# Kernel tuning notes

Measured on AMD Instinct MI355X. Metric: run time of the kernel, lower is better.

## Reference

```python
import jax, jax.numpy as jnp
import numpy as np

N = 50000      # nodes
E = 800000     # edges (before self loops)
IN = 128       # input feature dim
HID = 64       # hidden channels per head
H = 4          # heads
OUT = 1        # final out channels
D1 = H * HID   # 256, concat feature dim
NEG_SLOPE = 0.2


def _p(k, shape):
    return jax.random.normal(k, shape, jnp.float32) * 0.1


def setup_inputs() -> dict:
    key = jax.random.key(0)
    ks = jax.random.split(key, 32)
    inp = {
        "x": jax.random.normal(ks[0], (N, IN), jnp.float32),
        "edge_index": jax.random.randint(ks[1], (2, E), 0, N, dtype=jnp.int32),
        "batch": jnp.zeros((N,), jnp.int32),
    }
    # layer 0: GATConv(IN -> HID, heads=H, concat) ; Linear(IN -> H*HID)
    inp["cW0"] = _p(ks[2], (IN, H * HID)); inp["cas0"] = _p(ks[3], (H, HID))
    inp["cad0"] = _p(ks[4], (H, HID));     inp["cb0"] = jnp.zeros((D1,), jnp.float32)
    inp["lW0"] = _p(ks[5], (IN, D1));      inp["lb0"] = jnp.zeros((D1,), jnp.float32)
    # layer 1: GATConv(D1 -> HID, heads=H, concat) ; Linear(D1 -> D1)
    inp["cW1"] = _p(ks[6], (D1, H * HID)); inp["cas1"] = _p(ks[7], (H, HID))
    inp["cad1"] = _p(ks[8], (H, HID));     inp["cb1"] = jnp.zeros((D1,), jnp.float32)
    inp["lW1"] = _p(ks[9], (D1, D1));      inp["lb1"] = jnp.zeros((D1,), jnp.float32)
    # layer 2: GATConv(D1 -> OUT, heads=H, concat=False -> mean) ; Linear(D1 -> OUT)
    inp["cW2"] = _p(ks[10], (D1, H * OUT)); inp["cas2"] = _p(ks[11], (H, OUT))
    inp["cad2"] = _p(ks[12], (H, OUT));     inp["cb2"] = jnp.zeros((OUT,), jnp.float32)
    inp["lW2"] = _p(ks[13], (D1, OUT));     inp["lb2"] = jnp.zeros((OUT,), jnp.float32)
    return inp


def gat_conv(x, W, att_src, att_dst, bias, src, dst, out_c, concat):
    """PyG-style GATConv with self loops already included in (src, dst)."""
    n = x.shape[0]
    xl = (x @ W).reshape(n, H, out_c)                  # [N,H,C]
    a_s = (xl * att_src).sum(-1)                       # [N,H]
    a_d = (xl * att_dst).sum(-1)                       # [N,H]
    e = jax.nn.leaky_relu(a_s[src] + a_d[dst], NEG_SLOPE)   # [Et,H]
    # numerically stable segment softmax over destination nodes
    e_max = jax.ops.segment_max(e, dst, num_segments=n)
    ex = jnp.exp(e - e_max[dst])
    denom = jax.ops.segment_sum(ex, dst, num_segments=n)
    alpha = ex / (denom[dst] + 1e-16)                  # [Et,H]
    msg = xl[src] * alpha[..., None]                   # [Et,H,C]
    out = jax.ops.segment_sum(msg, dst, num_segments=n)  # [N,H,C]
    out = out.reshape(n, H * out_c) if concat else out.mean(axis=1)
    return out + bias


def _forward(x, edge_index,
             cW0, cas0, cad0, cb0, lW0, lb0,
             cW1, cas1, cad1, cb1, lW1, lb1,
             cW2, cas2, cad2, cb2, lW2, lb2):
    n = x.shape[0]
    loop = jnp.arange(n, dtype=edge_index.dtype)
    src = jnp.concatenate([edge_index[0], loop])
    dst = jnp.concatenate([edge_index[1], loop])
    h = jax.nn.elu(gat_conv(x, cW0, cas0, cad0, cb0, src, dst, HID, True) + (x @ lW0 + lb0))
    h = jax.nn.elu(gat_conv(h, cW1, cas1, cad1, cb1, src, dst, HID, True) + (h @ lW1 + lb1))
    return gat_conv(h, cW2, cas2, cad2, cb2, src, dst, OUT, False) + (h @ lW2 + lb2)


def reference(x, edge_index, batch,
              cW0, cas0, cad0, cb0, lW0, lb0,
              cW1, cas1, cad1, cb1, lW1, lb1,
              cW2, cas2, cad2, cb2, lW2, lb2):
    return _forward(x, edge_index,
                    cW0, cas0, cad0, cb0, lW0, lb0,
                    cW1, cas1, cad1, cb1, lW1, lb1,
                    cW2, cas2, cad2, cb2, lW2, lb2)
```

## Files before the change

kernel.cpp:

```cpp
#include <hip/hip_runtime.h>
#include <cstddef>
#include <cstdint>

#define NN 50000
#define EE 800000
#define ET_ (EE + NN)

typedef __attribute__((ext_vector_type(8))) short bf16x8;
typedef __attribute__((ext_vector_type(4))) float f32x4;

__device__ __forceinline__ float lrelu_(float x) { return x > 0.f ? x : 0.2f * x; }
__device__ __forceinline__ float elu_(float x)   { return x > 0.f ? x : (__expf(x) - 1.f); }
__device__ __forceinline__ short f2bf(float f) {
    unsigned u = __float_as_uint(f);
    unsigned r = (u + 0x7fffu + ((u >> 16) & 1u)) >> 16;
    return (short)r;
}
__device__ __forceinline__ float bflo(unsigned u) { return __uint_as_float(u << 16); }
__device__ __forceinline__ float bfhi(unsigned u) { return __uint_as_float(u & 0xffff0000u); }

#define GL16(gp, lp) __builtin_amdgcn_global_load_lds( \
    (const __attribute__((address_space(1))) unsigned int*)(gp), \
    (__attribute__((address_space(3))) unsigned int*)(lp), 16, 0, 0)


__global__ __launch_bounds__(256) void degree_k(const int* __restrict__ ei, int* __restrict__ deg) {
    int e = blockIdx.x * blockDim.x + threadIdx.x;
    if (e >= ET_) return;
    int d = (e < EE) ? ei[EE + e] : (e - EE);
    atomicAdd(&deg[d], 1);
}

__global__ __launch_bounds__(1024) void alloc_scan(const int* __restrict__ deg, int* __restrict__ rowptr,
                                                   int* __restrict__ gcnt, int n) {
    __shared__ int s[1024];
    __shared__ int basesh;
    int tid = threadIdx.x;
    int gid = blockIdx.x * 1024 + tid;
    int v = (gid < n) ? deg[gid] : 0;
    s[tid] = v;
    __syncthreads();
    for (int off = 1; off < 1024; off <<= 1) {
        int t = (tid >= off) ? s[tid - off] : 0;
        __syncthreads();
        s[tid] += t;
        __syncthreads();
    }
    if (tid == 1023) basesh = atomicAdd(gcnt, s[1023]);
    __syncthreads();
    if (gid < n) rowptr[gid] = basesh + s[tid] - v;
}

__global__ __launch_bounds__(256) void scatter_k(const int* __restrict__ ei,
                                                 const int* __restrict__ rowptr,
                                                 int* __restrict__ cursor,
                                                 int* __restrict__ csr_src) {
    int e = blockIdx.x * blockDim.x + threadIdx.x;
    if (e >= ET_) return;
    int s, d;
    if (e < EE) { s = ei[e]; d = ei[EE + e]; } else { s = e - EE; d = e - EE; }
    int pos = atomicAdd(&cursor[d], 1);
    csr_src[rowptr[d] + pos] = s;
}


__global__ __launch_bounds__(256) void prep_all(const float* __restrict__ x,
                                                const float* __restrict__ cW0, const float* __restrict__ lW0,
                                                const float* __restrict__ cW1, const float* __restrict__ lW1,
                                                short* __restrict__ xb, short* __restrict__ Wt0,
                                                short* __restrict__ Wt1) {
    int i = blockIdx.x * 256 + threadIdx.x;
    if (i < 1600000) {
        float4 v = *(const float4*)(x + (size_t)i * 4);
        short4 o;
        o.x = f2bf(v.x); o.y = f2bf(v.y); o.z = f2bf(v.z); o.w = f2bf(v.w);
        *(short4*)(xb + (size_t)i * 4) = o;
        return;
    }
    i -= 1600000;
    if (i < 512 * 128) {
        int n = i >> 7, k = i & 127;
        float v = (n < 256) ? cW0[k * 256 + n] : lW0[k * 256 + (n - 256)];
        Wt0[i] = f2bf(v);
        return;
    }
    i -= 512 * 128;
    if (i < 512 * 256) {
        int n = i >> 8, k = i & 255;
        float v = (n < 256) ? cW1[k * 256 + n] : lW1[k * 256 + (n - 256)];
        Wt1[i] = f2bf(v);
    }
}


__global__ __launch_bounds__(256) void gemm_bf16(const short* __restrict__ A,
                                                 const short* __restrict__ Wt,
                                                 const float* __restrict__ biasLin,
                                                 short* __restrict__ XLb,
                                                 short* __restrict__ Hlinb,
                                                 int M, int K) {
    __shared__ short As[128 * 32];
    __shared__ short Bs[128 * 32];
    const int tid = threadIdx.x;
    const int lane = tid & 63;
    const int wid = tid >> 6;
    const int bm = blockIdx.x * 128;
    const int col0 = blockIdx.y * 128;
    const int wr = wid >> 1, wc = wid & 1;

    f32x4 acc[4][4];
#pragma unroll
    for (int i = 0; i < 4; ++i)
#pragma unroll
        for (int j = 0; j < 4; ++j) acc[i][j] = (f32x4){0.f, 0.f, 0.f, 0.f};

    const int lrow = lane & 15, lk = lane >> 4;

    for (int k0 = 0; k0 < K; k0 += 32) {
#pragma unroll
        for (int it = 0; it < 2; ++it) {
            const int flat = tid + it * 256;
            const int row = flat >> 2, slot = flat & 3;
            const int ss = slot ^ (row & 3);
            int ar = bm + row; ar = (ar < M) ? ar : (M - 1);
            GL16(A + (size_t)ar * K + k0 + ss * 8, As + flat * 8);
            GL16(Wt + (size_t)(col0 + row) * K + k0 + ss * 8, Bs + flat * 8);
        }
        __syncthreads();
        bf16x8 af[4], bfr[4];
#pragma unroll
        for (int mi = 0; mi < 4; ++mi) {
            const int r = wr * 64 + mi * 16 + lrow;
            af[mi] = *(const bf16x8*)(As + (r * 4 + (lk ^ (r & 3))) * 8);
        }
#pragma unroll
        for (int ni = 0; ni < 4; ++ni) {
            const int c = wc * 64 + ni * 16 + lrow;
            bfr[ni] = *(const bf16x8*)(Bs + (c * 4 + (lk ^ (c & 3))) * 8);
        }
#pragma unroll
        for (int mi = 0; mi < 4; ++mi)
#pragma unroll
            for (int ni = 0; ni < 4; ++ni)
                acc[mi][ni] = __builtin_amdgcn_mfma_f32_16x16x32_bf16(af[mi], bfr[ni], acc[mi][ni], 0, 0, 0);
        __syncthreads();
    }

    const int lrow4 = (lane >> 4) * 4;
    const bool isLin = (col0 >= 256);
#pragma unroll
    for (int mi = 0; mi < 4; ++mi) {
#pragma unroll
        for (int ni = 0; ni < 4; ++ni) {
            const int col = col0 + wc * 64 + ni * 16 + (lane & 15);
#pragma unroll
            for (int rr = 0; rr < 4; ++rr) {
                const int grow = bm + wr * 64 + mi * 16 + lrow4 + rr;
                if (grow < M) {
                    float v = acc[mi][ni][rr];
                    if (isLin) {
                        const int c = col - 256;
                        Hlinb[(size_t)grow * 256 + c] = f2bf(v + biasLin[c]);
                    } else {
                        XLb[(size_t)grow * 256 + col] = f2bf(v);
                    }
                }
            }
        }
    }
}


__global__ __launch_bounds__(256) void attn_prep(const short* __restrict__ XLb,
                                                 const float* __restrict__ cas,
                                                 const float* __restrict__ cad,
                                                 float* __restrict__ AS,
                                                 float* __restrict__ AD, int n_nodes) {
    int n = (blockIdx.x * blockDim.x + threadIdx.x) >> 6;
    int lane = threadIdx.x & 63;
    if (n >= n_nodes) return;
    uint2 q = *(const uint2*)(XLb + (size_t)n * 256 + lane * 4);
    float x0 = bflo(q.x), x1 = bfhi(q.x);
    float x2 = bflo(q.y), x3 = bfhi(q.y);
    float4 sv = *(const float4*)(cas + lane * 4);
    float4 dv = *(const float4*)(cad + lane * 4);
    float ps = x0 * sv.x + x1 * sv.y + x2 * sv.z + x3 * sv.w;
    float pd = x0 * dv.x + x1 * dv.y + x2 * dv.z + x3 * dv.w;
#pragma unroll
    for (int off = 1; off < 16; off <<= 1) {
        ps += __shfl_xor(ps, off);
        pd += __shfl_xor(pd, off);
    }
    if ((lane & 15) == 0) {
        AS[n * 4 + (lane >> 4)] = ps;
        AD[n * 4 + (lane >> 4)] = pd;
    }
}


__global__ __launch_bounds__(256) void gat_agg(const short* __restrict__ XLb,
                                               const float* __restrict__ AS,
                                               const float* __restrict__ AD,
                                               const int* __restrict__ rowptr,
                                               const int* __restrict__ degarr,
                                               const int* __restrict__ csr_src,
                                               const float* __restrict__ cb,
                                               const short* __restrict__ Hlinb,
                                               short* __restrict__ Hb, int n_nodes) {
    __shared__ int   sIdx[4][64];
    __shared__ float sExT[4][4][72];

    const int tid = threadIdx.x;
    const int lane = tid & 63;
    const int w = tid >> 6;
    const int n = blockIdx.x * 4 + w;
    if (n >= n_nodes) return;

    const int rs = rowptr[n];
    const int deg = degarr[n];
    const float4 ad4 = *(const float4*)(AD + n * 4);

    float m0 = -1e30f, m1 = -1e30f, m2 = -1e30f, m3 = -1e30f;
    for (int base = 0; base < deg; base += 64) {
        int idx = base + lane;
        if (idx < deg) {
            int s = csr_src[rs + idx];
            float4 a = *(const float4*)(AS + s * 4);
            m0 = fmaxf(m0, lrelu_(a.x + ad4.x));
            m1 = fmaxf(m1, lrelu_(a.y + ad4.y));
            m2 = fmaxf(m2, lrelu_(a.z + ad4.z));
            m3 = fmaxf(m3, lrelu_(a.w + ad4.w));
        }
    }
#pragma unroll
    for (int off = 32; off > 0; off >>= 1) {
        m0 = fmaxf(m0, __shfl_xor(m0, off));
        m1 = fmaxf(m1, __shfl_xor(m1, off));
        m2 = fmaxf(m2, __shfl_xor(m2, off));
        m3 = fmaxf(m3, __shfl_xor(m3, off));
    }

    const int half = lane >> 5;
    const int l32 = lane & 31;
    const int ch0 = l32 * 8;
    const int h = l32 >> 3;

    float4 acc0 = make_float4(0.f, 0.f, 0.f, 0.f);
    float4 acc1 = make_float4(0.f, 0.f, 0.f, 0.f);
    float d0 = 0.f, d1 = 0.f, d2 = 0.f, d3 = 0.f;

    for (int base = 0; base < deg; base += 64) {
        int cnt = deg - base; if (cnt > 64) cnt = 64;
        int idx = base + lane;
        int sv = 0;
        float e0 = 0.f, e1 = 0.f, e2 = 0.f, e3 = 0.f;
        if (idx < deg) {
            sv = csr_src[rs + idx];
            float4 a = *(const float4*)(AS + sv * 4);
            e0 = __expf(lrelu_(a.x + ad4.x) - m0);
            e1 = __expf(lrelu_(a.y + ad4.y) - m1);
            e2 = __expf(lrelu_(a.z + ad4.z) - m2);
            e3 = __expf(lrelu_(a.w + ad4.w) - m3);
        }
        sIdx[w][lane] = sv;
        sExT[w][0][lane] = e0; sExT[w][1][lane] = e1;
        sExT[w][2][lane] = e2; sExT[w][3][lane] = e3;
        d0 += e0; d1 += e1; d2 += e2; d3 += e3;
        __builtin_amdgcn_wave_barrier();

        int cpad = (cnt + 1) & ~1;
        for (int j = 0; j < cpad; j += 2) {
            int jj = j + half;
            int s = sIdx[w][jj];
            float e = sExT[w][h][jj];
            const uint4 q = *(const uint4*)(XLb + (size_t)s * 256 + ch0);
            acc0.x += e * bflo(q.x); acc0.y += e * bfhi(q.x);
            acc0.z += e * bflo(q.y); acc0.w += e * bfhi(q.y);
            acc1.x += e * bflo(q.z); acc1.y += e * bfhi(q.z);
            acc1.z += e * bflo(q.w); acc1.w += e * bfhi(q.w);
        }
        __builtin_amdgcn_wave_barrier();
    }

    acc0.x += __shfl_xor(acc0.x, 32); acc0.y += __shfl_xor(acc0.y, 32);
    acc0.z += __shfl_xor(acc0.z, 32); acc0.w += __shfl_xor(acc0.w, 32);
    acc1.x += __shfl_xor(acc1.x, 32); acc1.y += __shfl_xor(acc1.y, 32);
    acc1.z += __shfl_xor(acc1.z, 32); acc1.w += __shfl_xor(acc1.w, 32);
#pragma unroll
    for (int off = 32; off > 0; off >>= 1) {
        d0 += __shfl_xor(d0, off); d1 += __shfl_xor(d1, off);
        d2 += __shfl_xor(d2, off); d3 += __shfl_xor(d3, off);
    }
    float den = (h == 0) ? d0 : (h == 1) ? d1 : (h == 2) ? d2 : d3;
    float inv = 1.f / (den + 1e-16f);

    if (lane < 32) {
        size_t o = (size_t)n * 256 + ch0;
        uint4 hq = *(const uint4*)(Hlinb + o);
        float4 cba = *(const float4*)(cb + ch0);
        float4 cbb = *(const float4*)(cb + ch0 + 4);
        float v0 = elu_(acc0.x * inv + cba.x + bflo(hq.x));
        float v1 = elu_(acc0.y * inv + cba.y + bfhi(hq.x));
        float v2 = elu_(acc0.z * inv + cba.z + bflo(hq.y));
        float v3 = elu_(acc0.w * inv + cba.w + bfhi(hq.y));
        float v4 = elu_(acc1.x * inv + cbb.x + bflo(hq.z));
        float v5 = elu_(acc1.y * inv + cbb.y + bfhi(hq.z));
        float v6 = elu_(acc1.z * inv + cbb.z + bflo(hq.w));
        float v7 = elu_(acc1.w * inv + cbb.w + bfhi(hq.w));
        uint4 ov;
        ov.x = (unsigned)(unsigned short)f2bf(v0) | ((unsigned)(unsigned short)f2bf(v1) << 16);
        ov.y = (unsigned)(unsigned short)f2bf(v2) | ((unsigned)(unsigned short)f2bf(v3) << 16);
        ov.z = (unsigned)(unsigned short)f2bf(v4) | ((unsigned)(unsigned short)f2bf(v5) << 16);
        ov.w = (unsigned)(unsigned short)f2bf(v6) | ((unsigned)(unsigned short)f2bf(v7) << 16);
        *(uint4*)(Hb + o) = ov;
    }
}


__global__ __launch_bounds__(256) void l2_prep(const short* __restrict__ Hin,
                                               const float* __restrict__ cW2,
                                               const float* __restrict__ lW2,
                                               const float* __restrict__ lb2,
                                               float* __restrict__ XL2,
                                               float* __restrict__ LIN2, int n_nodes) {
    int n = (blockIdx.x * blockDim.x + threadIdx.x) >> 6;
    int lane = threadIdx.x & 63;
    if (n >= n_nodes) return;
    uint2 q = *(const uint2*)(Hin + (size_t)n * 256 + lane * 4);
    float hk0 = bflo(q.x), hk1 = bfhi(q.x);
    float hk2 = bflo(q.y), hk3 = bfhi(q.y);
    int k = lane * 4;
    float4 w0 = *(const float4*)(cW2 + (k + 0) * 4);
    float4 w1 = *(const float4*)(cW2 + (k + 1) * 4);
    float4 w2 = *(const float4*)(cW2 + (k + 2) * 4);
    float4 w3 = *(const float4*)(cW2 + (k + 3) * 4);
    float a0 = hk0 * w0.x + hk1 * w1.x + hk2 * w2.x + hk3 * w3.x;
    float a1 = hk0 * w0.y + hk1 * w1.y + hk2 * w2.y + hk3 * w3.y;
    float a2 = hk0 * w0.z + hk1 * w1.z + hk2 * w2.z + hk3 * w3.z;
    float a3 = hk0 * w0.w + hk1 * w1.w + hk2 * w2.w + hk3 * w3.w;
    float4 lw = make_float4(lW2[k], lW2[k + 1], lW2[k + 2], lW2[k + 3]);
    float al = hk0 * lw.x + hk1 * lw.y + hk2 * lw.z + hk3 * lw.w;
#pragma unroll
    for (int off = 32; off > 0; off >>= 1) {
        a0 += __shfl_xor(a0, off); a1 += __shfl_xor(a1, off);
        a2 += __shfl_xor(a2, off); a3 += __shfl_xor(a3, off);
        al += __shfl_xor(al, off);
    }
    if (lane == 0) {
        float4 o = make_float4(a0, a1, a2, a3);
        *(float4*)(XL2 + n * 4) = o;
        LIN2[n] = al + lb2[0];
    }
}


__global__ __launch_bounds__(256) void l2_agg(const float* __restrict__ XL2,
                                              const float* __restrict__ LIN2,
                                              const float* __restrict__ cas2,
                                              const float* __restrict__ cad2,
                                              const float* __restrict__ cb2,
                                              const int* __restrict__ rowptr,
                                              const int* __restrict__ degarr,
                                              const int* __restrict__ csr_src,
                                              float* __restrict__ out, int n_nodes) {
    int n = (blockIdx.x * blockDim.x + threadIdx.x) >> 6;
    int lane = threadIdx.x & 63;
    if (n >= n_nodes) return;
    int rs = rowptr[n], re = rs + degarr[n];
    float4 xn = *(const float4*)(XL2 + n * 4);
    float cs0 = cas2[0], cs1 = cas2[1], cs2 = cas2[2], cs3 = cas2[3];
    float cd0 = cad2[0], cd1 = cad2[1], cd2 = cad2[2], cd3 = cad2[3];
    float ad0 = xn.x * cd0, ad1 = xn.y * cd1, ad2 = xn.z * cd2, ad3 = xn.w * cd3;

    float m0 = -1e30f, m1 = -1e30f, m2 = -1e30f, m3 = -1e30f;
    for (int i = rs + lane; i < re; i += 64) {
        int s = csr_src[i];
        float4 xs = *(const float4*)(XL2 + s * 4);
        m0 = fmaxf(m0, lrelu_(xs.x * cs0 + ad0));
        m1 = fmaxf(m1, lrelu_(xs.y * cs1 + ad1));
        m2 = fmaxf(m2, lrelu_(xs.z * cs2 + ad2));
        m3 = fmaxf(m3, lrelu_(xs.w * cs3 + ad3));
    }
#pragma unroll
    for (int off = 32; off > 0; off >>= 1) {
        m0 = fmaxf(m0, __shfl_xor(m0, off));
        m1 = fmaxf(m1, __shfl_xor(m1, off));
        m2 = fmaxf(m2, __shfl_xor(m2, off));
        m3 = fmaxf(m3, __shfl_xor(m3, off));
    }

    float d0 = 0.f, d1 = 0.f, d2 = 0.f, d3 = 0.f;
    float t0 = 0.f, t1 = 0.f, t2 = 0.f, t3 = 0.f;
    for (int i = rs + lane; i < re; i += 64) {
        int s = csr_src[i];
        float4 xs = *(const float4*)(XL2 + s * 4);
        float e0 = __expf(lrelu_(xs.x * cs0 + ad0) - m0);
        float e1 = __expf(lrelu_(xs.y * cs1 + ad1) - m1);
        float e2 = __expf(lrelu_(xs.z * cs2 + ad2) - m2);
        float e3 = __expf(lrelu_(xs.w * cs3 + ad3) - m3);
        d0 += e0; d1 += e1; d2 += e2; d3 += e3;
        t0 += e0 * xs.x; t1 += e1 * xs.y; t2 += e2 * xs.z; t3 += e3 * xs.w;
    }
#pragma unroll
    for (int off = 32; off > 0; off >>= 1) {
        d0 += __shfl_xor(d0, off); d1 += __shfl_xor(d1, off);
        d2 += __shfl_xor(d2, off); d3 += __shfl_xor(d3, off);
        t0 += __shfl_xor(t0, off); t1 += __shfl_xor(t1, off);
        t2 += __shfl_xor(t2, off); t3 += __shfl_xor(t3, off);
    }
    if (lane == 0) {
        float r = 0.25f * (t0 / (d0 + 1e-16f) + t1 / (d1 + 1e-16f) +
                           t2 / (d2 + 1e-16f) + t3 / (d3 + 1e-16f));
        out[n] = r + cb2[0] + LIN2[n];
    }
}


extern "C" void kernel_launch(void* const* d_in, const int* in_sizes, int n_in,
                              void* d_out, int out_size, void* d_ws, size_t ws_size,
                              hipStream_t stream) {
    const float* x    = (const float*)d_in[0];
    const int*   ei   = (const int*)d_in[1];
    const float* cW0  = (const float*)d_in[3];
    const float* cas0 = (const float*)d_in[4];
    const float* cad0 = (const float*)d_in[5];
    const float* cb0  = (const float*)d_in[6];
    const float* lW0  = (const float*)d_in[7];
    const float* lb0  = (const float*)d_in[8];
    const float* cW1  = (const float*)d_in[9];
    const float* cas1 = (const float*)d_in[10];
    const float* cad1 = (const float*)d_in[11];
    const float* cb1  = (const float*)d_in[12];
    const float* lW1  = (const float*)d_in[13];
    const float* lb1  = (const float*)d_in[14];
    const float* cW2  = (const float*)d_in[15];
    const float* cas2 = (const float*)d_in[16];
    const float* cad2 = (const float*)d_in[17];
    const float* cb2  = (const float*)d_in[18];
    const float* lW2  = (const float*)d_in[19];
    const float* lb2  = (const float*)d_in[20];
    float* out = (float*)d_out;

    short* xb    = (short*)d_ws;
    short* XLb   = xb + 6400000;
    short* HAb   = XLb + 12800000;
    short* HBb   = HAb + 12800000;
    short* Hlinb = HBb + 12800000;
    short* Wt0   = Hlinb + 12800000;
    short* Wt1   = Wt0 + 65536;
    float* AS    = (float*)(Wt1 + 131072);
    float* AD    = AS + 200000;
    float* XL2   = AD + 200000;
    float* LIN2  = XL2 + 200000;
    int* deg     = (int*)(LIN2 + NN);
    int* cursor  = deg + NN;
    int* gcnt    = cursor + NN;
    int* rowptr  = gcnt + 4;
    int* csr_src = rowptr + NN;

    dim3 b256(256);
    dim3 gEdges((ET_ + 255) / 256);
    dim3 gNodesWave((NN + 3) / 4);

    hipMemsetAsync(deg, 0, (2 * (size_t)NN + 4) * sizeof(int), stream);
    prep_all<<<dim3(7018), b256, 0, stream>>>(x, cW0, lW0, cW1, lW1, xb, Wt0, Wt1);
    degree_k<<<gEdges, b256, 0, stream>>>(ei, deg);
    alloc_scan<<<dim3((NN + 1023) / 1024), dim3(1024), 0, stream>>>(deg, rowptr, gcnt, NN);
    scatter_k<<<gEdges, b256, 0, stream>>>(ei, rowptr, cursor, csr_src);

    dim3 gemmGrid((NN + 127) / 128, 4);

    gemm_bf16<<<gemmGrid, b256, 0, stream>>>(xb, Wt0, lb0, XLb, Hlinb, NN, 128);
    attn_prep<<<gNodesWave, b256, 0, stream>>>(XLb, cas0, cad0, AS, AD, NN);
    gat_agg<<<gNodesWave, b256, 0, stream>>>(XLb, AS, AD, rowptr, deg, csr_src, cb0, Hlinb, HAb, NN);

    gemm_bf16<<<gemmGrid, b256, 0, stream>>>(HAb, Wt1, lb1, XLb, Hlinb, NN, 256);
    attn_prep<<<gNodesWave, b256, 0, stream>>>(XLb, cas1, cad1, AS, AD, NN);
    gat_agg<<<gNodesWave, b256, 0, stream>>>(XLb, AS, AD, rowptr, deg, csr_src, cb1, Hlinb, HBb, NN);

    l2_prep<<<gNodesWave, b256, 0, stream>>>(HBb, cW2, lW2, lb2, XL2, LIN2, NN);
    l2_agg<<<gNodesWave, b256, 0, stream>>>(XL2, LIN2, cas2, cad2, cb2, rowptr, deg, csr_src, out, NN);
}
```

Before: 511.4 us.

## Fuse layer-2 projection into aggregation, single-pass softmax, double-buffer GEMM

Three changes. The GEMM now double-buffers its LDS tiles, so the next K-slice loads while MFMAs run on the current one, and one barrier per iteration is dropped. gat_agg gains a fast path for nodes with degree at most 64 that reads neighbour indices and attention scores once and computes the max in registers instead of making two passes. The layer-2 projection (cW2/lW2 dot products) is fused into the second aggregation's epilogue, which removes the l2_prep kernel and the HBb bf16 write and re-read. The cost is extra LDS in the GEMM, which may lower occupancy, and extra branching and registers in gat_agg.

New measurement: 507.0 us. About the same (-0.9%).

```diff
diff --git a/kernel.cpp b/kernel.cpp
--- a/kernel.cpp
+++ b/kernel.cpp
@@ -99,8 +99,8 @@
                                                  short* __restrict__ XLb,
                                                  short* __restrict__ Hlinb,
                                                  int M, int K) {
-    __shared__ short As[128 * 32];
-    __shared__ short Bs[128 * 32];
+    __shared__ short As[2][128 * 32];
+    __shared__ short Bs[2][128 * 32];
     const int tid = threadIdx.x;
     const int lane = tid & 63;
     const int wid = tid >> 6;
@@ -116,34 +116,40 @@
 
     const int lrow = lane & 15, lk = lane >> 4;
 
-    for (int k0 = 0; k0 < K; k0 += 32) {
+    auto stage = [&](int b, int kk) {
 #pragma unroll
         for (int it = 0; it < 2; ++it) {
             const int flat = tid + it * 256;
             const int row = flat >> 2, slot = flat & 3;
             const int ss = slot ^ (row & 3);
             int ar = bm + row; ar = (ar < M) ? ar : (M - 1);
-            GL16(A + (size_t)ar * K + k0 + ss * 8, As + flat * 8);
-            GL16(Wt + (size_t)(col0 + row) * K + k0 + ss * 8, Bs + flat * 8);
-        }
+            GL16(A + (size_t)ar * K + kk + ss * 8, &As[b][flat * 8]);
+            GL16(Wt + (size_t)(col0 + row) * K + kk + ss * 8, &Bs[b][flat * 8]);
+        }
+    };
+
+    stage(0, 0);
+    int cur = 0;
+    for (int k0 = 0; k0 < K; k0 += 32) {
         __syncthreads();
+        if (k0 + 32 < K) stage(cur ^ 1, k0 + 32);
         bf16x8 af[4], bfr[4];
 #pragma unroll
         for (int mi = 0; mi < 4; ++mi) {
             const int r = wr * 64 + mi * 16 + lrow;
-            af[mi] = *(const bf16x8*)(As + (r * 4 + (lk ^ (r & 3))) * 8);
+            af[mi] = *(const bf16x8*)(&As[cur][(r * 4 + (lk ^ (r & 3))) * 8]);
         }
 #pragma unroll
         for (int ni = 0; ni < 4; ++ni) {
             const int c = wc * 64 + ni * 16 + lrow;
-            bfr[ni] = *(const bf16x8*)(Bs + (c * 4 + (lk ^ (c & 3))) * 8);
+            bfr[ni] = *(const bf16x8*)(&Bs[cur][(c * 4 + (lk ^ (c & 3))) * 8]);
         }
 #pragma unroll
         for (int mi = 0; mi < 4; ++mi)
 #pragma unroll
             for (int ni = 0; ni < 4; ++ni)
                 acc[mi][ni] = __builtin_amdgcn_mfma_f32_16x16x32_bf16(af[mi], bfr[ni], acc[mi][ni], 0, 0, 0);
-        __syncthreads();
+        cur ^= 1;
     }
 
     const int lrow4 = (lane >> 4) * 4;
@@ -206,7 +212,13 @@
                                                const int* __restrict__ csr_src,
                                                const float* __restrict__ cb,
                                                const short* __restrict__ Hlinb,
-                                               short* __restrict__ Hb, int n_nodes) {
+                                               short* __restrict__ Hb,
+                                               const float* __restrict__ cW2,
+                                               const float* __restrict__ lW2,
+                                               const float* __restrict__ lb2,
+                                               float* __restrict__ XL2,
+                                               float* __restrict__ LIN2,
+                                               int n_nodes) {
     __shared__ int   sIdx[4][64];
     __shared__ float sExT[4][4][72];
 
@@ -220,26 +232,6 @@
     const int deg = degarr[n];
     const float4 ad4 = *(const float4*)(AD + n * 4);
 
-    float m0 = -1e30f, m1 = -1e30f, m2 = -1e30f, m3 = -1e30f;
-    for (int base = 0; base < deg; base += 64) {
-        int idx = base + lane;
-        if (idx < deg) {
-            int s = csr_src[rs + idx];
-            float4 a = *(const float4*)(AS + s * 4);
-            m0 = fmaxf(m0, lrelu_(a.x + ad4.x));
-            m1 = fmaxf(m1, lrelu_(a.y + ad4.y));
-            m2 = fmaxf(m2, lrelu_(a.z + ad4.z));
-            m3 = fmaxf(m3, lrelu_(a.w + ad4.w));
-        }
-    }
-#pragma unroll
-    for (int off = 32; off > 0; off >>= 1) {
-        m0 = fmaxf(m0, __shfl_xor(m0, off));
-        m1 = fmaxf(m1, __shfl_xor(m1, off));
-        m2 = fmaxf(m2, __shfl_xor(m2, off));
-        m3 = fmaxf(m3, __shfl_xor(m3, off));
-    }
-
     const int half = lane >> 5;
     const int l32 = lane & 31;
     const int ch0 = l32 * 8;
@@ -249,26 +241,35 @@
     float4 acc1 = make_float4(0.f, 0.f, 0.f, 0.f);
     float d0 = 0.f, d1 = 0.f, d2 = 0.f, d3 = 0.f;
 
-    for (int base = 0; base < deg; base += 64) {
-        int cnt = deg - base; if (cnt > 64) cnt = 64;
-        int idx = base + lane;
+    if (deg <= 64) {
         int sv = 0;
+        float c0 = -1e30f, c1 = -1e30f, c2 = -1e30f, c3 = -1e30f;
+        if (lane < deg) {
+            sv = csr_src[rs + lane];
+            float4 a = *(const float4*)(AS + sv * 4);
+            c0 = lrelu_(a.x + ad4.x); c1 = lrelu_(a.y + ad4.y);
+            c2 = lrelu_(a.z + ad4.z); c3 = lrelu_(a.w + ad4.w);
+        }
+        float m0 = c0, m1 = c1, m2 = c2, m3 = c3;
+#pragma unroll
+        for (int off = 32; off > 0; off >>= 1) {
+            m0 = fmaxf(m0, __shfl_xor(m0, off));
+            m1 = fmaxf(m1, __shfl_xor(m1, off));
+            m2 = fmaxf(m2, __shfl_xor(m2, off));
+            m3 = fmaxf(m3, __shfl_xor(m3, off));
+        }
         float e0 = 0.f, e1 = 0.f, e2 = 0.f, e3 = 0.f;
-        if (idx < deg) {
-            sv = csr_src[rs + idx];
-            float4 a = *(const float4*)(AS + sv * 4);
-            e0 = __expf(lrelu_(a.x + ad4.x) - m0);
-            e1 = __expf(lrelu_(a.y + ad4.y) - m1);
-            e2 = __expf(lrelu_(a.z + ad4.z) - m2);
-            e3 = __expf(lrelu_(a.w + ad4.w) - m3);
+        if (lane < deg) {
+            e0 = __expf(c0 - m0); e1 = __expf(c1 - m1);
+            e2 = __expf(c2 - m2); e3 = __expf(c3 - m3);
         }
         sIdx[w][lane] = sv;
         sExT[w][0][lane] = e0; sExT[w][1][lane] = e1;
         sExT[w][2][lane] = e2; sExT[w][3][lane] = e3;
-        d0 += e0; d1 += e1; d2 += e2; d3 += e3;
+        d0 = e0; d1 = e1; d2 = e2; d3 = e3;
         __builtin_amdgcn_wave_barrier();
 
-        int cpad = (cnt + 1) & ~1;
+        int cpad = (deg + 1) & ~1;
         for (int j = 0; j < cpad; j += 2) {
             int jj = j + half;
             int s = sIdx[w][jj];
@@ -279,7 +280,57 @@
             acc1.x += e * bflo(q.z); acc1.y += e * bfhi(q.z);
             acc1.z += e * bflo(q.w); acc1.w += e * bfhi(q.w);
         }
-        __builtin_amdgcn_wave_barrier();
+    } else {
+        float m0 = -1e30f, m1 = -1e30f, m2 = -1e30f, m3 = -1e30f;
+        for (int base = 0; base < deg; base += 64) {
+            int idx = base + lane;
+            if (idx < deg) {
+                int s = csr_src[rs + idx];
+                float4 a = *(const float4*)(AS + s * 4);
+                m0 = fmaxf(m0, lrelu_(a.x + ad4.x));
+                m1 = fmaxf(m1, lrelu_(a.y + ad4.y));
+                m2 = fmaxf(m2, lrelu_(a.z + ad4.z));
+                m3 = fmaxf(m3, lrelu_(a.w + ad4.w));
+            }
+        }
+#pragma unroll
+        for (int off = 32; off > 0; off >>= 1) {
+            m0 = fmaxf(m0, __shfl_xor(m0, off));
+            m1 = fmaxf(m1, __shfl_xor(m1, off));
+            m2 = fmaxf(m2, __shfl_xor(m2, off));
+            m3 = fmaxf(m3, __shfl_xor(m3, off));
+        }
+        for (int base = 0; base < deg; base += 64) {
+            int cnt = deg - base; if (cnt > 64) cnt = 64;
+            int idx = base + lane;
+            int sv = 0;
+            float e0 = 0.f, e1 = 0.f, e2 = 0.f, e3 = 0.f;
+            if (idx < deg) {
+                sv = csr_src[rs + idx];
+                float4 a = *(const float4*)(AS + sv * 4);
+                e0 = __expf(lrelu_(a.x + ad4.x) - m0);
+                e1 = __expf(lrelu_(a.y + ad4.y) - m1);
+                e2 = __expf(lrelu_(a.z + ad4.z) - m2);
+                e3 = __expf(lrelu_(a.w + ad4.w) - m3);
+            }
+            sIdx[w][lane] = sv;
+            sExT[w][0][lane] = e0; sExT[w][1][lane] = e1;
+            sExT[w][2][lane] = e2; sExT[w][3][lane] = e3;
+            d0 += e0; d1 += e1; d2 += e2; d3 += e3;
+            __builtin_amdgcn_wave_barrier();
+            int cpad = (cnt + 1) & ~1;
+            for (int j = 0; j < cpad; j += 2) {
+                int jj = j + half;
+                int s = sIdx[w][jj];
+                float e = sExT[w][h][jj];
+                const uint4 q = *(const uint4*)(XLb + (size_t)s * 256 + ch0);
+                acc0.x += e * bflo(q.x); acc0.y += e * bfhi(q.x);
+                acc0.z += e * bflo(q.y); acc0.w += e * bfhi(q.y);
+                acc1.x += e * bflo(q.z); acc1.y += e * bfhi(q.z);
+                acc1.z += e * bflo(q.w); acc1.w += e * bfhi(q.w);
+            }
+            __builtin_amdgcn_wave_barrier();
+        }
     }
 
     acc0.x += __shfl_xor(acc0.x, 32); acc0.y += __shfl_xor(acc0.y, 32);
@@ -294,62 +345,55 @@
     float den = (h == 0) ? d0 : (h == 1) ? d1 : (h == 2) ? d2 : d3;
     float inv = 1.f / (den + 1e-16f);
 
+    float v0 = 0.f, v1 = 0.f, v2 = 0.f, v3 = 0.f, v4 = 0.f, v5 = 0.f, v6 = 0.f, v7 = 0.f;
     if (lane < 32) {
         size_t o = (size_t)n * 256 + ch0;
         uint4 hq = *(const uint4*)(Hlinb + o);
         float4 cba = *(const float4*)(cb + ch0);
         float4 cbb = *(const float4*)(cb + ch0 + 4);
-        float v0 = elu_(acc0.x * inv + cba.x + bflo(hq.x));
-        float v1 = elu_(acc0.y * inv + cba.y + bfhi(hq.x));
-        float v2 = elu_(acc0.z * inv + cba.z + bflo(hq.y));
-        float v3 = elu_(acc0.w * inv + cba.w + bfhi(hq.y));
-        float v4 = elu_(acc1.x * inv + cbb.x + bflo(hq.z));
-        float v5 = elu_(acc1.y * inv + cbb.y + bfhi(hq.z));
-        float v6 = elu_(acc1.z * inv + cbb.z + bflo(hq.w));
-        float v7 = elu_(acc1.w * inv + cbb.w + bfhi(hq.w));
+        v0 = elu_(acc0.x * inv + cba.x + bflo(hq.x));
+        v1 = elu_(acc0.y * inv + cba.y + bfhi(hq.x));
+        v2 = elu_(acc0.z * inv + cba.z + bflo(hq.y));
+        v3 = elu_(acc0.w * inv + cba.w + bfhi(hq.y));
+        v4 = elu_(acc1.x * inv + cbb.x + bflo(hq.z));
+        v5 = elu_(acc1.y * inv + cbb.y + bfhi(hq.z));
+        v6 = elu_(acc1.z * inv + cbb.z + bflo(hq.w));
+        v7 = elu_(acc1.w * inv + cbb.w + bfhi(hq.w));
+    }
+
+    if (XL2 != nullptr) {
+        float p0 = 0.f, p1 = 0.f, p2 = 0.f, p3 = 0.f, pl = 0.f;
+        if (lane < 32) {
+            const float vv[8] = {v0, v1, v2, v3, v4, v5, v6, v7};
+            float4 lwa = *(const float4*)(lW2 + ch0);
+            float4 lwb = *(const float4*)(lW2 + ch0 + 4);
+            const float lw[8] = {lwa.x, lwa.y, lwa.z, lwa.w, lwb.x, lwb.y, lwb.z, lwb.w};
+#pragma unroll
+            for (int j = 0; j < 8; ++j) {
+                float4 wv = *(const float4*)(cW2 + (ch0 + j) * 4);
+                p0 += vv[j] * wv.x; p1 += vv[j] * wv.y;
+                p2 += vv[j] * wv.z; p3 += vv[j] * wv.w;
+                pl += vv[j] * lw[j];
+            }
+        }
+#pragma unroll
+        for (int off = 16; off > 0; off >>= 1) {
+            p0 += __shfl_xor(p0, off); p1 += __shfl_xor(p1, off);
+            p2 += __shfl_xor(p2, off); p3 += __shfl_xor(p3, off);
+            pl += __shfl_xor(pl, off);
+        }
+        if (lane == 0) {
+            *(float4*)(XL2 + n * 4) = make_float4(p0, p1, p2, p3);
+            LIN2[n] = pl + lb2[0];
+        }
+    } else if (lane < 32) {
+        size_t o = (size_t)n * 256 + ch0;
         uint4 ov;
         ov.x = (unsigned)(unsigned short)f2bf(v0) | ((unsigned)(unsigned short)f2bf(v1) << 16);
         ov.y = (unsigned)(unsigned short)f2bf(v2) | ((unsigned)(unsigned short)f2bf(v3) << 16);
         ov.z = (unsigned)(unsigned short)f2bf(v4) | ((unsigned)(unsigned short)f2bf(v5) << 16);
         ov.w = (unsigned)(unsigned short)f2bf(v6) | ((unsigned)(unsigned short)f2bf(v7) << 16);
         *(uint4*)(Hb + o) = ov;
-    }
-}
-
-
-__global__ __launch_bounds__(256) void l2_prep(const short* __restrict__ Hin,
-                                               const float* __restrict__ cW2,
-                                               const float* __restrict__ lW2,
-                                               const float* __restrict__ lb2,
-                                               float* __restrict__ XL2,
-                                               float* __restrict__ LIN2, int n_nodes) {
-    int n = (blockIdx.x * blockDim.x + threadIdx.x) >> 6;
-    int lane = threadIdx.x & 63;
-    if (n >= n_nodes) return;
-    uint2 q = *(const uint2*)(Hin + (size_t)n * 256 + lane * 4);
-    float hk0 = bflo(q.x), hk1 = bfhi(q.x);
-    float hk2 = bflo(q.y), hk3 = bfhi(q.y);
-    int k = lane * 4;
-    float4 w0 = *(const float4*)(cW2 + (k + 0) * 4);
-    float4 w1 = *(const float4*)(cW2 + (k + 1) * 4);
-    float4 w2 = *(const float4*)(cW2 + (k + 2) * 4);
-    float4 w3 = *(const float4*)(cW2 + (k + 3) * 4);
-    float a0 = hk0 * w0.x + hk1 * w1.x + hk2 * w2.x + hk3 * w3.x;
-    float a1 = hk0 * w0.y + hk1 * w1.y + hk2 * w2.y + hk3 * w3.y;
-    float a2 = hk0 * w0.z + hk1 * w1.z + hk2 * w2.z + hk3 * w3.z;
-    float a3 = hk0 * w0.w + hk1 * w1.w + hk2 * w2.w + hk3 * w3.w;
-    float4 lw = make_float4(lW2[k], lW2[k + 1], lW2[k + 2], lW2[k + 3]);
-    float al = hk0 * lw.x + hk1 * lw.y + hk2 * lw.z + hk3 * lw.w;
-#pragma unroll
-    for (int off = 32; off > 0; off >>= 1) {
-        a0 += __shfl_xor(a0, off); a1 += __shfl_xor(a1, off);
-        a2 += __shfl_xor(a2, off); a3 += __shfl_xor(a3, off);
-        al += __shfl_xor(al, off);
-    }
-    if (lane == 0) {
-        float4 o = make_float4(a0, a1, a2, a3);
-        *(float4*)(XL2 + n * 4) = o;
-        LIN2[n] = al + lb2[0];
     }
 }
 
@@ -444,8 +488,7 @@
     short* xb    = (short*)d_ws;
     short* XLb   = xb + 6400000;
     short* HAb   = XLb + 12800000;
-    short* HBb   = HAb + 12800000;
-    short* Hlinb = HBb + 12800000;
+    short* Hlinb = HAb + 12800000;
     short* Wt0   = Hlinb + 12800000;
     short* Wt1   = Wt0 + 65536;
     float* AS    = (float*)(Wt1 + 131072);
@@ -472,12 +515,13 @@
 
     gemm_bf16<<<gemmGrid, b256, 0, stream>>>(xb, Wt0, lb0, XLb, Hlinb, NN, 128);
     attn_prep<<<gNodesWave, b256, 0, stream>>>(XLb, cas0, cad0, AS, AD, NN);
-    gat_agg<<<gNodesWave, b256, 0, stream>>>(XLb, AS, AD, rowptr, deg, csr_src, cb0, Hlinb, HAb, NN);
+    gat_agg<<<gNodesWave, b256, 0, stream>>>(XLb, AS, AD, rowptr, deg, csr_src, cb0, Hlinb,
+                                             HAb, nullptr, nullptr, nullptr, nullptr, nullptr, NN);
 
     gemm_bf16<<<gemmGrid, b256, 0, stream>>>(HAb, Wt1, lb1, XLb, Hlinb, NN, 256);
     attn_prep<<<gNodesWave, b256, 0, stream>>>(XLb, cas1, cad1, AS, AD, NN);
-    gat_agg<<<gNodesWave, b256, 0, stream>>>(XLb, AS, AD, rowptr, deg, csr_src, cb1, Hlinb, HBb, NN);
-
-    l2_prep<<<gNodesWave, b256, 0, stream>>>(HBb, cW2, lW2, lb2, XL2, LIN2, NN);
+    gat_agg<<<gNodesWave, b256, 0, stream>>>(XLb, AS, AD, rowptr, deg, csr_src, cb1, Hlinb,
+                                             nullptr, cW2, lW2, lb2, XL2, LIN2, NN);
+
     l2_agg<<<gNodesWave, b256, 0, stream>>>(XL2, LIN2, cas2, cad2, cb2, rowptr, deg, csr_src, out, NN);
 }
```
